# Performance work log

Measured on AMD Instinct MI355X. Metric: run time of the kernel, lower is better.

## Reference

```python
import jax, jax.numpy as jnp
import numpy as np

NUM_CLASSES = 10
EPS = 1e-6


def setup_inputs() -> dict:
    key = jax.random.key(0)
    kx, ky, k1, k2, k3, k4 = jax.random.split(key, 6)
    B, N, F = 64, 4096, 256
    hidden, out_dim = 64, 128
    return {
        "X_support": jax.random.normal(kx, (B, N, F), dtype=jnp.float32),
        "y_support": jax.random.randint(ky, (B, N), 0, NUM_CLASSES, dtype=jnp.int64),
        "W1": jax.random.normal(k1, (6, hidden), dtype=jnp.float32) * 0.4,
        "b1": jax.random.normal(k2, (hidden,), dtype=jnp.float32) * 0.02,
        "W2": jax.random.normal(k3, (hidden, out_dim), dtype=jnp.float32) * 0.12,
        "b2": jax.random.normal(k4, (out_dim,), dtype=jnp.float32) * 0.02,
    }


def _stats(X, y):
    # X: [B, N, F] float, y: [B, N] int labels in [0, NUM_CLASSES)
    B, N, F = X.shape
    missing_rate = jnp.isnan(X).astype(jnp.float32).mean(axis=1)        # [B, F]
    cleaned = jnp.nan_to_num(X, nan=0.0)                                # [B, N, F]

    # unique ratio per column: count distinct via sorted adjacent diffs
    srt = jnp.sort(cleaned, axis=1)
    uniq = 1.0 + (jnp.diff(srt, axis=1) != 0).astype(jnp.float32).sum(axis=1)  # [B, F]
    unique_ratio = uniq / max(1, N)

    mean = cleaned.mean(axis=1)                                         # [B, F]
    variance = cleaned.var(axis=1)                                      # [B, F] (unbiased=False)
    mean_abs = jnp.abs(cleaned).mean(axis=1)
    max_abs = jnp.abs(cleaned).max(axis=1)

    # classification target score: between-class variance / overall variance
    onehot = jax.nn.one_hot(y, NUM_CLASSES, dtype=jnp.float32)          # [B, N, C]
    counts = onehot.sum(axis=1)                                         # [B, C]
    class_sums = jnp.einsum("bnc,bnf->bcf", onehot, cleaned)            # [B, C, F]
    class_means = class_sums / jnp.maximum(counts, 1.0)[:, :, None]     # [B, C, F] (0 for empty class)
    dev2 = jnp.square(class_means - mean[:, None, :])                   # [B, C, F]
    between_var = jnp.einsum("bc,bcf->bf", counts, dev2) / jnp.maximum(counts.sum(axis=1), 1.0)[:, None]
    overall_var = jnp.maximum(variance, EPS)
    target_score = between_var / overall_var                            # [B, F]

    stats = jnp.stack(
        [target_score, missing_rate, unique_ratio, variance, mean_abs, max_abs], axis=-1
    )  # [B, F, 6]
    return jnp.nan_to_num(stats, nan=0.0, posinf=0.0, neginf=0.0)


def reference(X_support, y_support, W1, b1, W2, b2):
    stats = _stats(X_support, y_support)                                # [B, F, 6]
    h = jax.nn.gelu(stats @ W1 + b1, approximate=False)
    return h @ W2 + b2                                                  # [B, F, output_dim]
```

## Files before the change

kernel.cpp:

```cpp
#include <hip/hip_runtime.h>
#include <math.h>

#define NB 64
#define NN 4096
#define NF 256
#define NC 10
#define NSPLIT 16
#define CH 256
#define LW 263
#define EMPTYK 0xFFFFFFFFu

__global__ __launch_bounds__(256, 4) void k_stats(const float* __restrict__ X,
                                                  const int* __restrict__ Y,
                                                  unsigned* __restrict__ XT,
                                                  float* __restrict__ P) {
  __shared__ unsigned ldsT[32 * LW];
  const int bi = blockIdx.x;
  const int b = bi >> 4, sp = bi & 15;
  const int t = threadIdx.x;
  const int w = t >> 6, l = t & 63;
  const int n0 = sp * CH;
  const float4* Xv = (const float4*)X;

  const int y0 = Y[b * NN + n0 + l];
  const int y1 = Y[b * NN + n0 + 64 + l];
  const int y2 = Y[b * NN + n0 + 128 + l];
  const int y3 = Y[b * NN + n0 + 192 + l];

  float s1 = 0.f, s2 = 0.f, sab = 0.f, mab = 0.f;
  float cls[NC] = {};
  float nanc4[4] = {0.f, 0.f, 0.f, 0.f};

  const int colbase = 4 * l + (l >> 3);
  const int myoff = t + (t >> 5);

  float4 pf[8];
#pragma unroll
  for (int it = 0; it < 8; ++it) {
    const int n = n0 + it * 4 + w;
    pf[it] = Xv[(size_t)(b * NN + n) * (NF / 4) + l];
  }

  for (int tile = 0; tile < 8; ++tile) {
#pragma unroll
    for (int it = 0; it < 8; ++it) {
      const float v[4] = {pf[it].x, pf[it].y, pf[it].z, pf[it].w};
      const int lb = (it * 4 + w) * LW + colbase;
#pragma unroll
      for (int q = 0; q < 4; ++q) {
        float c = v[q];
        if (c != c) { nanc4[q] += 1.f; c = 0.f; }
        ldsT[lb + q] = (c == 0.f) ? 0u : __float_as_uint(c);
      }
    }
    __syncthreads();

    if (tile < 7) {
#pragma unroll
      for (int it = 0; it < 8; ++it) {
        const int n = n0 + (tile + 1) * 32 + it * 4 + w;
        pf[it] = Xv[(size_t)(b * NN + n) * (NF / 4) + l];
      }
    }

#pragma unroll
    for (int j = 0; j < 8; ++j) {
      const int idx = t + 256 * j;
      const int f = idx >> 3, rr4 = idx & 7;
      const int fo = f + (f >> 5);
      uint4 o;
      o.x = ldsT[(rr4 * 4 + 0) * LW + fo];
      o.y = ldsT[(rr4 * 4 + 1) * LW + fo];
      o.z = ldsT[(rr4 * 4 + 2) * LW + fo];
      o.w = ldsT[(rr4 * 4 + 3) * LW + fo];
      ((uint4*)(XT + (size_t)(b * NF + f) * NN + n0 + tile * 32))[rr4] = o;
    }

    const int kk = tile >> 1;
    const int yl = (kk & 2) ? ((kk & 1) ? y3 : y2) : ((kk & 1) ? y1 : y0);
    const int lbase = (tile & 1) * 32;
#pragma unroll
    for (int r = 0; r < 32; ++r) {
      const float c = __uint_as_float(ldsT[r * LW + myoff]);
      const int y = __builtin_amdgcn_readlane(yl, lbase + r);
      s1 += c;
      s2 = fmaf(c, c, s2);
      const float a = fabsf(c);
      sab += a;
      mab = fmaxf(mab, a);
      switch (y) {
        case 0: cls[0] += c; break; case 1: cls[1] += c; break;
        case 2: cls[2] += c; break; case 3: cls[3] += c; break;
        case 4: cls[4] += c; break; case 5: cls[5] += c; break;
        case 6: cls[6] += c; break; case 7: cls[7] += c; break;
        case 8: cls[8] += c; break; case 9: cls[9] += c; break;
        default: break;
      }
    }
    __syncthreads();
  }

  float* nl = (float*)ldsT;
#pragma unroll
  for (int q = 0; q < 4; ++q) nl[w * 256 + 4 * l + q] = nanc4[q];
  __syncthreads();
  const float nanc = nl[t] + nl[256 + t] + nl[512 + t] + nl[768 + t];

  float vals[16];
  vals[0] = s1; vals[1] = s2; vals[2] = sab; vals[3] = mab; vals[4] = nanc;
#pragma unroll
  for (int c = 0; c < NC; ++c) vals[5 + c] = cls[c];
  vals[15] = 0.f;
  float4* Pv = (float4*)(P + ((size_t)(b * NSPLIT + sp) * NF + t) * 16);
  Pv[0] = *(float4*)&vals[0];
  Pv[1] = *(float4*)&vals[4];
  Pv[2] = *(float4*)&vals[8];
  Pv[3] = *(float4*)&vals[12];
}

__global__ __launch_bounds__(256) void k_uniq(const unsigned* __restrict__ XT,
                                              unsigned* __restrict__ uniq) {
  __shared__ unsigned tab[8192];
  const int t = threadIdx.x;
  const size_t base = (size_t)blockIdx.x * NN;

  const uint4* Xv = (const uint4*)(XT + base);
  uint4 kv0 = Xv[t], kv1 = Xv[256 + t], kv2 = Xv[512 + t], kv3 = Xv[768 + t];

  uint4* tv = (uint4*)tab;
  const uint4 e4 = make_uint4(EMPTYK, EMPTYK, EMPTYK, EMPTYK);
#pragma unroll
  for (int i = 0; i < 8; ++i) tv[t + 256 * i] = e4;

  unsigned key[16] = {kv0.x, kv0.y, kv0.z, kv0.w, kv1.x, kv1.y, kv1.z, kv1.w,
                      kv2.x, kv2.y, kv2.z, kv2.w, kv3.x, kv3.y, kv3.z, kv3.w};
  unsigned h[16];
#pragma unroll
  for (int q = 0; q < 16; ++q) h[q] = (key[q] * 2654435761u) >> 19;
  unsigned pend = 0xFFFFu;
  unsigned salt = 0x9E3779B9u;
  int cnt = 0;
  __syncthreads();

  while (true) {
#pragma unroll
    for (int q = 0; q < 16; ++q)
      if (pend & (1u << q)) tab[h[q]] = key[q];
    __syncthreads();
#pragma unroll
    for (int q = 0; q < 16; ++q)
      if (pend & (1u << q)) {
        if (tab[h[q]] == key[q]) pend &= ~(1u << q);
        else h[q] = ((key[q] ^ salt) * 2654435761u) >> 19;
      }
    salt += 0x9E3779B9u;
    const int live = __syncthreads_count(pend != 0);
#pragma unroll
    for (int i = 0; i < 8; ++i) {
      uint4 v = tv[t + 256 * i];
      cnt += (v.x != EMPTYK) + (v.y != EMPTYK) + (v.z != EMPTYK) + (v.w != EMPTYK);
      if (live) tv[t + 256 * i] = e4;
    }
    if (!live) break;
    __syncthreads();
  }

  for (int off = 32; off; off >>= 1) cnt += __shfl_down(cnt, off, 64);
  __syncthreads();
  if ((t & 63) == 0) tab[t >> 6] = (unsigned)cnt;
  __syncthreads();
  if (t == 0) uniq[blockIdx.x] = tab[0] + tab[1] + tab[2] + tab[3];
}

__global__ __launch_bounds__(256) void k_finalize(const float* __restrict__ P,
                                                  const int* __restrict__ Y,
                                                  const unsigned* __restrict__ uniq,
                                                  float* __restrict__ stats6) {
  __shared__ float whist[4 * NC];
  const int b = blockIdx.x;
  const int t = threadIdx.x;

  int cnt[NC];
#pragma unroll
  for (int c = 0; c < NC; ++c) cnt[c] = 0;
#pragma unroll
  for (int i = 0; i < 16; ++i) {
    const int y = Y[b * NN + 256 * i + t];
#pragma unroll
    for (int c = 0; c < NC; ++c) cnt[c] += (y == c) ? 1 : 0;
  }
#pragma unroll
  for (int c = 0; c < NC; ++c) {
    int v = cnt[c];
    for (int off = 32; off; off >>= 1) v += __shfl_down(v, off, 64);
    cnt[c] = v;
  }
  if ((t & 63) == 0) {
#pragma unroll
    for (int c = 0; c < NC; ++c) whist[(t >> 6) * NC + c] = (float)cnt[c];
  }
  __syncthreads();

  const int f = t;
  const int col = b * 256 + f;
  float acc[16];
#pragma unroll
  for (int i = 0; i < 16; ++i) acc[i] = 0.f;
  for (int sp = 0; sp < NSPLIT; ++sp) {
    const float4* p4 = (const float4*)(P + ((size_t)(b * NSPLIT + sp) * NF + f) * 16);
    float4 A = p4[0], B4 = p4[1], C4 = p4[2], D4 = p4[3];
    acc[0] += A.x; acc[1] += A.y; acc[2] += A.z; acc[3] = fmaxf(acc[3], A.w);
    acc[4] += B4.x; acc[5] += B4.y; acc[6] += B4.z; acc[7] += B4.w;
    acc[8] += C4.x; acc[9] += C4.y; acc[10] += C4.z; acc[11] += C4.w;
    acc[12] += D4.x; acc[13] += D4.y; acc[14] += D4.z;
  }
  const float invN = 1.f / (float)NN;
  const float mean = acc[0] * invN;
  float var = acc[1] * invN - mean * mean;
  if (var < 0.f) var = 0.f;
  const float meanabs = acc[2] * invN;
  const float maxabs = acc[3];
  const float miss = acc[4] * invN;
  const float uratio = (float)uniq[col] * invN;
  float btw = 0.f;
#pragma unroll
  for (int c = 0; c < NC; ++c) {
    const float cntc = whist[c] + whist[NC + c] + whist[2 * NC + c] + whist[3 * NC + c];
    const float m = acc[5 + c] / fmaxf(cntc, 1.f);
    const float d = m - mean;
    btw = fmaf(cntc * d, d, btw);
  }
  btw *= invN;
  const float target = btw / fmaxf(var, 1e-6f);
  float st[6] = {target, miss, uratio, var, meanabs, maxabs};
#pragma unroll
  for (int i = 0; i < 6; ++i)
    if (!(fabsf(st[i]) <= 3.4028235e38f)) st[i] = 0.f;
#pragma unroll
  for (int i = 0; i < 6; ++i) stats6[(size_t)col * 6 + i] = st[i];
}

__global__ __launch_bounds__(256) void k_mlp(const float* __restrict__ stats6,
                                             const float* __restrict__ W1,
                                             const float* __restrict__ b1,
                                             const float* __restrict__ W2,
                                             const float* __restrict__ b2,
                                             float* __restrict__ out) {
  __shared__ float w1s[6 * 64];
  __shared__ float b1s[64];
  __shared__ float w2s[64 * 128];
  __shared__ float b2s[128];
  __shared__ float sts[32 * 6];
  __shared__ float hs[64 * 36];
  const int t = threadIdx.x;
  const int cb0 = blockIdx.x * 32;
  for (int i = t; i < 96; i += 256) ((float4*)w1s)[i] = ((const float4*)W1)[i];
  if (t < 64) b1s[t] = b1[t];
  for (int i = t; i < 2048; i += 256) ((float4*)w2s)[i] = ((const float4*)W2)[i];
  if (t < 128) b2s[t] = b2[t];
  if (t < 48) ((float4*)sts)[t] = ((const float4*)(stats6 + (size_t)cb0 * 6))[t];
  __syncthreads();

  const int k = t & 63, cg = t >> 6;
#pragma unroll
  for (int cc = 0; cc < 8; ++cc) {
    const int col = cg + 4 * cc;
    float pre = b1s[k];
#pragma unroll
    for (int s = 0; s < 6; ++s) pre = fmaf(sts[col * 6 + s], w1s[s * 64 + k], pre);
    const float h = 0.5f * pre * (1.f + erff(pre * 0.70710678118654752f));
    hs[k * 36 + col] = h;
  }
  __syncthreads();

  const int j4 = (t & 31) * 4, c4 = (t >> 5) * 4;
  float4 a[4];
  const float4 bj = *(const float4*)&b2s[j4];
  a[0] = bj; a[1] = bj; a[2] = bj; a[3] = bj;
  for (int kk = 0; kk < 64; ++kk) {
    const float4 wv = *(const float4*)&w2s[kk * 128 + j4];
    const float4 hv = *(const float4*)&hs[kk * 36 + c4];
    const float hc[4] = {hv.x, hv.y, hv.z, hv.w};
#pragma unroll
    for (int ci = 0; ci < 4; ++ci) {
      a[ci].x = fmaf(hc[ci], wv.x, a[ci].x);
      a[ci].y = fmaf(hc[ci], wv.y, a[ci].y);
      a[ci].z = fmaf(hc[ci], wv.z, a[ci].z);
      a[ci].w = fmaf(hc[ci], wv.w, a[ci].w);
    }
  }
#pragma unroll
  for (int ci = 0; ci < 4; ++ci) {
    const int col = cb0 + c4 + ci;
    *(float4*)&out[(size_t)col * 128 + j4] = a[ci];
  }
}

extern "C" void kernel_launch(void* const* d_in, const int* in_sizes, int n_in,
                              void* d_out, int out_size, void* d_ws, size_t ws_size,
                              hipStream_t stream) {
  const float* X = (const float*)d_in[0];
  const int* Y = (const int*)d_in[1];
  const float* W1 = (const float*)d_in[2];
  const float* b1 = (const float*)d_in[3];
  const float* W2 = (const float*)d_in[4];
  const float* b2 = (const float*)d_in[5];
  float* out = (float*)d_out;

  char* w = (char*)d_ws;
  unsigned* XT = (unsigned*)w;
  float* P = (float*)(w + 268435456ull);
  float* stats6 = (float*)(w + 285212672ull);
  unsigned* uniq = (unsigned*)(w + 285608448ull);

  k_stats<<<NB * NSPLIT, 256, 0, stream>>>(X, Y, XT, P);
  k_uniq<<<NB * NF, 256, 0, stream>>>(XT, uniq);
  k_finalize<<<NB, 256, 0, stream>>>(P, Y, uniq, stats6);
  k_mlp<<<512, 256, 0, stream>>>(stats6, W1, b1, W2, b2, out);
}
```

Measured before the change: 596.8 us.

## Count unique keys with per-slot tag election instead of table scans

The LDS hash table used to count distinct values per column drops the per-round clear and full-table scan of non-empty slots. Instead, each matched key writes its owner id into a 16-bit tag array, and only the thread whose tag survives increments the count. The table also shrinks from 8192 to 4096 slots, which cuts LDS use and may raise occupancy. The trade-off is that a fuller table can need more collision rounds.

```diff
diff --git a/kernel.cpp b/kernel.cpp
--- a/kernel.cpp
+++ b/kernel.cpp
@@ -8,7 +8,7 @@
 #define NSPLIT 16
 #define CH 256
 #define LW 263
-#define EMPTYK 0xFFFFFFFFu
+#define USLOTS 4096
 
 __global__ __launch_bounds__(256, 4) void k_stats(const float* __restrict__ X,
                                                   const int* __restrict__ Y,
@@ -120,53 +120,50 @@
 
 __global__ __launch_bounds__(256) void k_uniq(const unsigned* __restrict__ XT,
                                               unsigned* __restrict__ uniq) {
-  __shared__ unsigned tab[8192];
+  __shared__ unsigned tab[USLOTS];
+  __shared__ unsigned short tag[USLOTS];
   const int t = threadIdx.x;
   const size_t base = (size_t)blockIdx.x * NN;
 
   const uint4* Xv = (const uint4*)(XT + base);
   uint4 kv0 = Xv[t], kv1 = Xv[256 + t], kv2 = Xv[512 + t], kv3 = Xv[768 + t];
-
-  uint4* tv = (uint4*)tab;
-  const uint4 e4 = make_uint4(EMPTYK, EMPTYK, EMPTYK, EMPTYK);
-#pragma unroll
-  for (int i = 0; i < 8; ++i) tv[t + 256 * i] = e4;
 
   unsigned key[16] = {kv0.x, kv0.y, kv0.z, kv0.w, kv1.x, kv1.y, kv1.z, kv1.w,
                       kv2.x, kv2.y, kv2.z, kv2.w, kv3.x, kv3.y, kv3.z, kv3.w};
   unsigned h[16];
 #pragma unroll
-  for (int q = 0; q < 16; ++q) h[q] = (key[q] * 2654435761u) >> 19;
+  for (int q = 0; q < 16; ++q) h[q] = (key[q] * 2654435761u) >> 20;
   unsigned pend = 0xFFFFu;
   unsigned salt = 0x9E3779B9u;
   int cnt = 0;
-  __syncthreads();
 
   while (true) {
 #pragma unroll
     for (int q = 0; q < 16; ++q)
       if (pend & (1u << q)) tab[h[q]] = key[q];
     __syncthreads();
+    unsigned match = 0;
 #pragma unroll
     for (int q = 0; q < 16; ++q)
       if (pend & (1u << q)) {
-        if (tab[h[q]] == key[q]) pend &= ~(1u << q);
-        else h[q] = ((key[q] ^ salt) * 2654435761u) >> 19;
+        if (tab[h[q]] == key[q]) {
+          match |= (1u << q);
+          tag[h[q]] = (unsigned short)(t * 16 + q);
+        } else {
+          h[q] = ((key[q] ^ salt) * 2654435761u) >> 20;
+        }
       }
     salt += 0x9E3779B9u;
-    const int live = __syncthreads_count(pend != 0);
-#pragma unroll
-    for (int i = 0; i < 8; ++i) {
-      uint4 v = tv[t + 256 * i];
-      cnt += (v.x != EMPTYK) + (v.y != EMPTYK) + (v.z != EMPTYK) + (v.w != EMPTYK);
-      if (live) tv[t + 256 * i] = e4;
-    }
-    if (!live) break;
     __syncthreads();
+#pragma unroll
+    for (int q = 0; q < 16; ++q)
+      if (match & (1u << q))
+        cnt += (tag[h[q]] == (unsigned short)(t * 16 + q)) ? 1 : 0;
+    pend &= ~match;
+    if (__syncthreads_count(pend != 0) == 0) break;
   }
 
   for (int off = 32; off; off >>= 1) cnt += __shfl_down(cnt, off, 64);
-  __syncthreads();
   if ((t & 63) == 0) tab[t >> 6] = (unsigned)cnt;
   __syncthreads();
   if (t == 0) uniq[blockIdx.x] = tab[0] + tab[1] + tab[2] + tab[3];
```

Measured after the change: 582.0 us. 1.03x faster.
